# Performance work log

Measured on AMD Instinct MI355X. Metric: run time of the kernel, lower is better.

## Reference

```python
import jax, jax.numpy as jnp
import numpy as np

K = 512   # codebook entries per group (num_embeddings // 4)
D = 128   # dim per group (embedding_dim // 4)
BETA = 0.25


def setup_inputs() -> dict:
    key = jax.random.key(0)
    k0, k1, k2, k3, k4 = jax.random.split(key, 5)
    latents = jax.random.normal(k0, (16, 2048, 512), dtype=jnp.float32)
    scale = 1.0 / K
    w1 = jax.random.uniform(k1, (K, D), dtype=jnp.float32, minval=-scale, maxval=scale)
    w2 = jax.random.uniform(k2, (K, D), dtype=jnp.float32, minval=-scale, maxval=scale)
    w3 = jax.random.uniform(k3, (K, D), dtype=jnp.float32, minval=-scale, maxval=scale)
    w4 = jax.random.uniform(k4, (K, D), dtype=jnp.float32, minval=-scale, maxval=scale)
    return {"latents": latents, "w1": w1, "w2": w2, "w3": w3, "w4": w4}


def _vq(latents, w1, w2, w3, w4):
    B, S, E = latents.shape
    # Slicing [:, :, g*D:(g+1)*D] is equivalent to reshape into groups.
    x = latents.reshape(B, S, 4, D)                    # [B,S,4,D]
    W = jnp.stack([w1, w2, w3, w4], axis=0)            # [4,K,D]
    x_sq = jnp.sum(x * x, axis=-1, keepdims=True)      # [B,S,4,1]
    w_sq = jnp.sum(W * W, axis=-1)                     # [4,K]
    cross = jnp.einsum('bsgd,gkd->bsgk', x, W)         # [B,S,4,K]
    dist = x_sq + w_sq[None, None, :, :] - 2.0 * cross
    idx = jnp.argmin(dist, axis=-1)                    # [B,S,4]
    g_idx = jnp.arange(4)[None, None, :]
    q = W[g_idx, idx]                                  # [B,S,4,D]
    # per-group MSE losses (mean over B,S,D)
    sg = jax.lax.stop_gradient
    commit = jnp.mean((sg(q) - x) ** 2, axis=(0, 1, 3))   # [4]
    embed = jnp.mean((q - sg(x)) ** 2, axis=(0, 1, 3))    # [4]
    vq_loss = jnp.sum(BETA * commit + embed)
    # straight-through estimator
    q_st = x + sg(q - x)
    return q_st.reshape(B, S, E), vq_loss


def reference(latents, w1, w2, w3, w4):
    return _vq(latents, w1, w2, w3, w4)
```

## Files before the change

kernel.cpp:

```cpp
#include <hip/hip_runtime.h>
#include <stdint.h>

typedef __attribute__((ext_vector_type(8))) short short8;
typedef __attribute__((ext_vector_type(4))) float f32x4;

static __device__ __forceinline__ short f2bf(float f) {
    union { float f; uint32_t u; } v; v.f = f;
    uint32_t u = v.u;
    return (short)((u + 0x7FFFu + ((u >> 16) & 1u)) >> 16);
}

static __device__ __forceinline__ void gload_lds16(const void* g, void* l) {
    __builtin_amdgcn_global_load_lds(
        (const __attribute__((address_space(1))) unsigned int*)g,
        (__attribute__((address_space(3))) unsigned int*)l, 16, 0, 0);
}


__global__ void vq_prep_kernel(const float* __restrict__ w0, const float* __restrict__ w1,
                               const float* __restrict__ w2, const float* __restrict__ w3,
                               float* __restrict__ ws) {
    int tid = blockIdx.x * blockDim.x + threadIdx.x;
    const float* wg = (tid < 512) ? w0 : (tid < 1024) ? w1 : (tid < 1536) ? w2 : w3;
    int c  = tid & 511;
    int g  = tid >> 9;
    int nt = c >> 4, lr = c & 15;
    const float* src = wg + (size_t)c * 128;
    char* cb = (char*)ws + 65536 + (size_t)g * 131072;
    float s = 0.f;
    #pragma unroll
    for (int cg = 0; cg < 16; cg++) {
        int ks = cg >> 2, lh = cg & 3;
        float4 v0 = *(const float4*)(src + cg * 8);
        float4 v1 = *(const float4*)(src + cg * 8 + 4);
        s += v0.x*v0.x + v0.y*v0.y + v0.z*v0.z + v0.w*v0.w
           + v1.x*v1.x + v1.y*v1.y + v1.z*v1.z + v1.w*v1.w;
        short8 b;
        b[0] = f2bf(v0.x); b[1] = f2bf(v0.y); b[2] = f2bf(v0.z); b[3] = f2bf(v0.w);
        b[4] = f2bf(v1.x); b[5] = f2bf(v1.y); b[6] = f2bf(v1.z); b[7] = f2bf(v1.w);
        *(short8*)(cb + ((size_t)((nt * 4 + ks) * 64 + lh * 16 + lr) * 16)) = b;
    }
    ws[64 + tid] = -0.5f * s;
}

__global__ __launch_bounds__(512, 4)
void vq_main_kernel(const float* __restrict__ lat,
                    const float* __restrict__ w0, const float* __restrict__ w1,
                    const float* __restrict__ w2, const float* __restrict__ w3,
                    float* __restrict__ out, float* __restrict__ ws) {
    __shared__ __align__(16) short lw[32768];
    __shared__ float lwsq[512];
    __shared__ float slsum[8];

    const int bid   = blockIdx.x;
    const int g     = bid >> 7;
    const int tbase = (bid & 127) * 256;
    const float* wg = (g == 0) ? w0 : (g == 1) ? w1 : (g == 2) ? w2 : w3;
    const char* cbg = (const char*)ws + 65536 + (size_t)g * 131072;

    const int t    = threadIdx.x;
    const int wave = t >> 6;
    const int l    = t & 63;
    const int lr   = l & 15;
    const int lh   = l >> 4;

    lwsq[t] = ws[64 + g * 512 + t];

    {
        const char* gsrc = cbg + wave * 8192 + l * 16;
        char* ldst = (char*)lw + wave * 8192;
        #pragma unroll
        for (int j = 0; j < 8; j++)
            gload_lds16(gsrc + j * 1024, ldst + j * 1024);
    }

    short8 afrag[2][4];
    float  xsq[2];
    const int wtok = tbase + wave * 32;
    #pragma unroll
    for (int mt = 0; mt < 2; mt++) {
        int token = wtok + mt * 16 + lr;
        const float* xp = lat + (size_t)token * 512 + g * 128 + lh * 8;
        float part = 0.f;
        #pragma unroll
        for (int ks = 0; ks < 4; ks++) {
            float4 v0 = *(const float4*)(xp + ks * 32);
            float4 v1 = *(const float4*)(xp + ks * 32 + 4);
            part += v0.x*v0.x + v0.y*v0.y + v0.z*v0.z + v0.w*v0.w
                  + v1.x*v1.x + v1.y*v1.y + v1.z*v1.z + v1.w*v1.w;
            short8 a;
            a[0] = f2bf(v0.x); a[1] = f2bf(v0.y); a[2] = f2bf(v0.z); a[3] = f2bf(v0.w);
            a[4] = f2bf(v1.x); a[5] = f2bf(v1.y); a[6] = f2bf(v1.z); a[7] = f2bf(v1.w);
            afrag[mt][ks] = a;
        }
        part += __shfl_xor(part, 16);
        part += __shfl_xor(part, 32);
        xsq[mt] = part;
    }

    float runmax[8];
    int   runidx[8];
    #pragma unroll
    for (int i = 0; i < 8; i++) { runmax[i] = -3.4e38f; runidx[i] = 0; }

    const char* lwb = (const char*)lw + l * 16;

    #pragma unroll
    for (int h = 0; h < 2; h++) {
        __syncthreads();

        short8 b0 = *(const short8*)(lwb);
        short8 b1 = *(const short8*)(lwb + 1024);
        short8 b2 = *(const short8*)(lwb + 2048);
        short8 b3 = *(const short8*)(lwb + 3072);
        #pragma unroll 2
        for (int nt = 0; nt < 16; nt++) {
            short8 c0 = b0, c1 = b1, c2 = b2, c3 = b3;
            const char* nbase = lwb + ((nt + 1) & 15) * 4096;
            b0 = *(const short8*)(nbase);
            b1 = *(const short8*)(nbase + 1024);
            b2 = *(const short8*)(nbase + 2048);
            b3 = *(const short8*)(nbase + 3072);
            int  gnt  = h * 16 + nt;
            float hn  = lwsq[gnt * 16 + lr];
            int  code = gnt * 16 + lr;
            #pragma unroll
            for (int mt = 0; mt < 2; mt++) {
                f32x4 acc = {hn, hn, hn, hn};
                acc = __builtin_amdgcn_mfma_f32_16x16x32_bf16(afrag[mt][0], c0, acc, 0, 0, 0);
                acc = __builtin_amdgcn_mfma_f32_16x16x32_bf16(afrag[mt][1], c1, acc, 0, 0, 0);
                acc = __builtin_amdgcn_mfma_f32_16x16x32_bf16(afrag[mt][2], c2, acc, 0, 0, 0);
                acc = __builtin_amdgcn_mfma_f32_16x16x32_bf16(afrag[mt][3], c3, acc, 0, 0, 0);
                #pragma unroll
                for (int r = 0; r < 4; r++) {
                    int i = mt * 4 + r;
                    float s = acc[r];
                    if (s > runmax[i]) { runmax[i] = s; runidx[i] = code; }
                }
            }
        }

        if (h == 0) {
            __syncthreads();
            const char* gsrc = cbg + 65536 + wave * 8192 + l * 16;
            char* ldst = (char*)lw + wave * 8192;
            #pragma unroll
            for (int j = 0; j < 8; j++)
                gload_lds16(gsrc + j * 1024, ldst + j * 1024);
        }
    }

    #pragma unroll
    for (int i = 0; i < 8; i++) {
        float v = runmax[i]; int id = runidx[i];
        #pragma unroll
        for (int m = 1; m < 16; m <<= 1) {
            float ov = __shfl_xor(v, m);
            int   oi = __shfl_xor(id, m);
            if (ov > v || (ov == v && oi < id)) { v = ov; id = oi; }
        }
        runmax[i] = v; runidx[i] = id;
    }

    float lsum = 0.f;
    #pragma unroll
    for (int mt = 0; mt < 2; mt++) {
        #pragma unroll
        for (int r = 0; r < 4; r++) {
            int row = lh * 4 + r;
            float xs = __shfl(xsq[mt], (l & 48) | row);
            if (lr == 0) lsum += xs - 2.f * runmax[mt * 4 + r];
        }
    }
    lsum += __shfl_xor(lsum, 16);
    lsum += __shfl_xor(lsum, 32);
    if (l == 0) slsum[wave] = lsum;
    __syncthreads();
    if (t == 0) {
        float s = 0.f;
        #pragma unroll
        for (int i = 0; i < 8; i++) s += slsum[i];
        ws[4096 + bid] = s;
    }

    #pragma unroll
    for (int it = 0; it < 16; it++) {
        const int j0 = it * 2, j1 = it * 2 + 1;
        int idx0 = __shfl(runidx[((j0 >> 4) << 2) | (j0 & 3)], ((j0 >> 2) & 3) << 4);
        int idx1 = __shfl(runidx[((j1 >> 4) << 2) | (j1 & 3)], ((j1 >> 2) & 3) << 4);
        int idx  = (l >= 32) ? idx1 : idx0;
        int tloc = it * 2 + (l >> 5);
        int col  = (l & 31) * 4;
        float4 v = *(const float4*)(wg + (size_t)idx * 128 + col);
        *(float4*)(out + (size_t)(wtok + tloc) * 512 + g * 128 + col) = v;
    }
}

__global__ void vq_finalize_kernel(const float* __restrict__ ws, float* __restrict__ out) {
    __shared__ float s8[8];
    float v = ws[4096 + threadIdx.x];
    #pragma unroll
    for (int m = 1; m < 64; m <<= 1) v += __shfl_xor(v, m);
    if ((threadIdx.x & 63) == 0) s8[threadIdx.x >> 6] = v;
    __syncthreads();
    if (threadIdx.x == 0) {
        float s = 0.f;
        #pragma unroll
        for (int i = 0; i < 8; i++) s += s8[i];
        out[16777216] = 1.25f * s * (1.0f / 4194304.0f);
    }
}

extern "C" void kernel_launch(void* const* d_in, const int* in_sizes, int n_in,
                              void* d_out, int out_size, void* d_ws, size_t ws_size,
                              hipStream_t stream) {
    const float* lat = (const float*)d_in[0];
    const float* w1  = (const float*)d_in[1];
    const float* w2  = (const float*)d_in[2];
    const float* w3  = (const float*)d_in[3];
    const float* w4  = (const float*)d_in[4];
    float* out = (float*)d_out;
    float* ws  = (float*)d_ws;

    vq_prep_kernel<<<8, 256, 0, stream>>>(w1, w2, w3, w4, ws);
    vq_main_kernel<<<512, 512, 0, stream>>>(lat, w1, w2, w3, w4, out, ws);
    vq_finalize_kernel<<<1, 512, 0, stream>>>(ws, out);
}
```

Before: 47.48 us.

## Pack score and index into one key, double tokens per wave, deepen prefetch

```diff
diff --git a/kernel.cpp b/kernel.cpp
--- a/kernel.cpp
+++ b/kernel.cpp
@@ -3,6 +3,8 @@
 
 typedef __attribute__((ext_vector_type(8))) short short8;
 typedef __attribute__((ext_vector_type(4))) float f32x4;
+
+#define BIG 4.0f
 
 static __device__ __forceinline__ short f2bf(float f) {
     union { float f; uint32_t u; } v; v.f = f;
@@ -40,17 +42,17 @@
         b[4] = f2bf(v1.x); b[5] = f2bf(v1.y); b[6] = f2bf(v1.z); b[7] = f2bf(v1.w);
         *(short8*)(cb + ((size_t)((nt * 4 + ks) * 64 + lh * 16 + lr) * 16)) = b;
     }
-    ws[64 + tid] = -0.5f * s;
-}
-
-__global__ __launch_bounds__(512, 4)
+    ws[64 + tid] = BIG - 0.5f * s;
+}
+
+__global__ __launch_bounds__(256, 2)
 void vq_main_kernel(const float* __restrict__ lat,
                     const float* __restrict__ w0, const float* __restrict__ w1,
                     const float* __restrict__ w2, const float* __restrict__ w3,
                     float* __restrict__ out, float* __restrict__ ws) {
     __shared__ __align__(16) short lw[32768];
     __shared__ float lwsq[512];
-    __shared__ float slsum[8];
+    __shared__ float slsum[4];
 
     const int bid   = blockIdx.x;
     const int g     = bid >> 7;
@@ -63,22 +65,24 @@
     const int l    = t & 63;
     const int lr   = l & 15;
     const int lh   = l >> 4;
-
-    lwsq[t] = ws[64 + g * 512 + t];
+    const uint32_t invlr = 511 - lr;
+
+    lwsq[t]       = ws[64 + g * 512 + t];
+    lwsq[t + 256] = ws[64 + g * 512 + t + 256];
 
     {
-        const char* gsrc = cbg + wave * 8192 + l * 16;
-        char* ldst = (char*)lw + wave * 8192;
-        #pragma unroll
-        for (int j = 0; j < 8; j++)
+        const char* gsrc = cbg + wave * 16384 + l * 16;
+        char* ldst = (char*)lw + wave * 16384;
+        #pragma unroll
+        for (int j = 0; j < 16; j++)
             gload_lds16(gsrc + j * 1024, ldst + j * 1024);
     }
 
-    short8 afrag[2][4];
-    float  xsq[2];
-    const int wtok = tbase + wave * 32;
-    #pragma unroll
-    for (int mt = 0; mt < 2; mt++) {
+    short8 afrag[4][4];
+    float  xsq[4];
+    const int wtok = tbase + wave * 64;
+    #pragma unroll
+    for (int mt = 0; mt < 4; mt++) {
         int token = wtok + mt * 16 + lr;
         const float* xp = lat + (size_t)token * 512 + g * 128 + lh * 8;
         float part = 0.f;
@@ -98,10 +102,9 @@
         xsq[mt] = part;
     }
 
-    float runmax[8];
-    int   runidx[8];
-    #pragma unroll
-    for (int i = 0; i < 8; i++) { runmax[i] = -3.4e38f; runidx[i] = 0; }
+    uint32_t runkey[16];
+    #pragma unroll
+    for (int i = 0; i < 16; i++) runkey[i] = 0u;
 
     const char* lwb = (const char*)lw + l * 16;
 
@@ -109,23 +112,34 @@
     for (int h = 0; h < 2; h++) {
         __syncthreads();
 
-        short8 b0 = *(const short8*)(lwb);
-        short8 b1 = *(const short8*)(lwb + 1024);
-        short8 b2 = *(const short8*)(lwb + 2048);
-        short8 b3 = *(const short8*)(lwb + 3072);
+        short8 bf[2][4];
+        float  hv[2];
+        #pragma unroll
+        for (int p = 0; p < 2; p++) {
+            const char* base = lwb + p * 4096;
+            bf[p][0] = *(const short8*)(base);
+            bf[p][1] = *(const short8*)(base + 1024);
+            bf[p][2] = *(const short8*)(base + 2048);
+            bf[p][3] = *(const short8*)(base + 3072);
+            hv[p] = lwsq[(h * 16 + p) * 16 + lr];
+        }
+
         #pragma unroll 2
         for (int nt = 0; nt < 16; nt++) {
-            short8 c0 = b0, c1 = b1, c2 = b2, c3 = b3;
-            const char* nbase = lwb + ((nt + 1) & 15) * 4096;
-            b0 = *(const short8*)(nbase);
-            b1 = *(const short8*)(nbase + 1024);
-            b2 = *(const short8*)(nbase + 2048);
-            b3 = *(const short8*)(nbase + 3072);
-            int  gnt  = h * 16 + nt;
-            float hn  = lwsq[gnt * 16 + lr];
-            int  code = gnt * 16 + lr;
+            const int cur = nt & 1;
+            short8 c0 = bf[cur][0], c1 = bf[cur][1], c2 = bf[cur][2], c3 = bf[cur][3];
+            float  hn = hv[cur];
+            {
+                const char* nbase = lwb + ((nt + 2) & 15) * 4096;
+                bf[cur][0] = *(const short8*)(nbase);
+                bf[cur][1] = *(const short8*)(nbase + 1024);
+                bf[cur][2] = *(const short8*)(nbase + 2048);
+                bf[cur][3] = *(const short8*)(nbase + 3072);
+                hv[cur] = lwsq[(h * 16 + ((nt + 2) & 15)) * 16 + lr];
+            }
+            const uint32_t invc = invlr - (uint32_t)((h * 16 + nt) * 16);
             #pragma unroll
-            for (int mt = 0; mt < 2; mt++) {
+            for (int mt = 0; mt < 4; mt++) {
                 f32x4 acc = {hn, hn, hn, hn};
                 acc = __builtin_amdgcn_mfma_f32_16x16x32_bf16(afrag[mt][0], c0, acc, 0, 0, 0);
                 acc = __builtin_amdgcn_mfma_f32_16x16x32_bf16(afrag[mt][1], c1, acc, 0, 0, 0);
@@ -133,58 +147,56 @@
                 acc = __builtin_amdgcn_mfma_f32_16x16x32_bf16(afrag[mt][3], c3, acc, 0, 0, 0);
                 #pragma unroll
                 for (int r = 0; r < 4; r++) {
+                    uint32_t key = (__float_as_uint(acc[r]) & 0xFFFFFE00u) | invc;
                     int i = mt * 4 + r;
-                    float s = acc[r];
-                    if (s > runmax[i]) { runmax[i] = s; runidx[i] = code; }
+                    runkey[i] = max(runkey[i], key);
                 }
             }
         }
 
         if (h == 0) {
             __syncthreads();
-            const char* gsrc = cbg + 65536 + wave * 8192 + l * 16;
-            char* ldst = (char*)lw + wave * 8192;
+            const char* gsrc = cbg + 65536 + wave * 16384 + l * 16;
+            char* ldst = (char*)lw + wave * 16384;
             #pragma unroll
-            for (int j = 0; j < 8; j++)
+            for (int j = 0; j < 16; j++)
                 gload_lds16(gsrc + j * 1024, ldst + j * 1024);
         }
     }
 
     #pragma unroll
-    for (int i = 0; i < 8; i++) {
-        float v = runmax[i]; int id = runidx[i];
-        #pragma unroll
-        for (int m = 1; m < 16; m <<= 1) {
-            float ov = __shfl_xor(v, m);
-            int   oi = __shfl_xor(id, m);
-            if (ov > v || (ov == v && oi < id)) { v = ov; id = oi; }
-        }
-        runmax[i] = v; runidx[i] = id;
-    }
-
+    for (int i = 0; i < 16; i++) {
+        uint32_t k = runkey[i];
+        k = max(k, (uint32_t)__shfl_xor((int)k, 1));
+        k = max(k, (uint32_t)__shfl_xor((int)k, 2));
+        k = max(k, (uint32_t)__shfl_xor((int)k, 4));
+        k = max(k, (uint32_t)__shfl_xor((int)k, 8));
+        runkey[i] = k;
+    }
+
+    int runidx[16];
     float lsum = 0.f;
     #pragma unroll
-    for (int mt = 0; mt < 2; mt++) {
+    for (int mt = 0; mt < 4; mt++) {
         #pragma unroll
         for (int r = 0; r < 4; r++) {
+            int i = mt * 4 + r;
+            uint32_t k = runkey[i];
+            runidx[i] = 511 - (int)(k & 0x1FFu);
+            float val = __uint_as_float(k & 0xFFFFFE00u);
             int row = lh * 4 + r;
             float xs = __shfl(xsq[mt], (l & 48) | row);
-            if (lr == 0) lsum += xs - 2.f * runmax[mt * 4 + r];
+            if (lr == 0) lsum += xs + 2.f * BIG - 2.f * val;
         }
     }
     lsum += __shfl_xor(lsum, 16);
     lsum += __shfl_xor(lsum, 32);
     if (l == 0) slsum[wave] = lsum;
     __syncthreads();
-    if (t == 0) {
-        float s = 0.f;
-        #pragma unroll
-        for (int i = 0; i < 8; i++) s += slsum[i];
-        ws[4096 + bid] = s;
-    }
-
-    #pragma unroll
-    for (int it = 0; it < 16; it++) {
+    if (t == 0) ws[4096 + bid] = slsum[0] + slsum[1] + slsum[2] + slsum[3];
+
+    #pragma unroll
+    for (int it = 0; it < 32; it++) {
         const int j0 = it * 2, j1 = it * 2 + 1;
         int idx0 = __shfl(runidx[((j0 >> 4) << 2) | (j0 & 3)], ((j0 >> 2) & 3) << 4);
         int idx1 = __shfl(runidx[((j1 >> 4) << 2) | (j1 & 3)], ((j1 >> 2) & 3) << 4);
@@ -223,6 +235,6 @@
     float* ws  = (float*)d_ws;
 
     vq_prep_kernel<<<8, 256, 0, stream>>>(w1, w2, w3, w4, ws);
-    vq_main_kernel<<<512, 512, 0, stream>>>(lat, w1, w2, w3, w4, out, ws);
+    vq_main_kernel<<<512, 256, 0, stream>>>(lat, w1, w2, w3, w4, out, ws);
     vq_finalize_kernel<<<1, 512, 0, stream>>>(ws, out);
 }
```

Result: no change. 47.55 us (+0.2%).
